# Kernel tuning notes

Hardware: AMD Instinct MI355X
Metric: run time of the kernel (lower is better)

The kernel has to match this reference:

```python
import jax, jax.numpy as jnp
import numpy as np

INPUT_DIM = 512
EMBED_DIM = 512
N_HEAD = 8
HEAD_DIM = EMBED_DIM // N_HEAD


def setup_inputs() -> dict:
    key = jax.random.key(0)
    k0, k1, k2 = jax.random.split(key, 3)
    B, S = 2, 4096
    X = jax.random.normal(k0, (B, S, INPUT_DIM), dtype=jnp.float32)
    # xavier_uniform for Linear weights (torch weight shape [out, in])
    def xavier(k, out_f, in_f):
        bound = float(np.sqrt(6.0 / (in_f + out_f)))
        return jax.random.uniform(k, (out_f, in_f), jnp.float32, -bound, bound)
    W_qkv = xavier(k1, 3 * EMBED_DIM, INPUT_DIM)
    b_qkv = jnp.zeros((3 * EMBED_DIM,), jnp.float32)
    W_o = xavier(k2, EMBED_DIM, EMBED_DIM)
    b_o = jnp.zeros((EMBED_DIM,), jnp.float32)
    return {"X": X, "W_qkv": W_qkv, "b_qkv": b_qkv, "W_o": W_o, "b_o": b_o}


def reference(X, W_qkv, b_qkv, W_o, b_o):
    B, S, _ = X.shape
    # fused QKV projection: [B,S,3E]
    qkv = jnp.einsum("bsd,ed->bse", X, W_qkv) + b_qkv
    # [B,S,H,3*hd] -> [B,H,S,3*hd]
    qkv = qkv.reshape(B, S, N_HEAD, 3 * HEAD_DIM).transpose(0, 2, 1, 3)
    q, k, v = jnp.split(qkv, 3, axis=-1)
    scale = 1.0 / jnp.sqrt(jnp.asarray(HEAD_DIM, q.dtype))
    logits = jnp.einsum("bhqd,bhkd->bhqk", q, k) * scale  # [B,H,S,S]
    attn = jax.nn.softmax(logits, axis=-1)
    vals = jnp.einsum("bhqk,bhkd->bhqd", attn, v)
    vals = vals.transpose(0, 2, 1, 3).reshape(B, S, EMBED_DIM)
    out = jnp.einsum("bse,fe->bsf", vals, W_o) + b_o
    return out
```

## Files before the change

kernel.cpp:

```cpp
#include <hip/hip_runtime.h>

#define S_   4096
#define D_IN 512
#define E_   512
#define HD   64

typedef __attribute__((ext_vector_type(8))) short short8;
typedef __attribute__((ext_vector_type(16))) float f32x16;

#define MFMA32(a, b, c) __builtin_amdgcn_mfma_f32_32x32x16_bf16((a), (b), (c), 0, 0, 0)

__device__ __forceinline__ unsigned short f2bf(float f) {
  unsigned u = __builtin_bit_cast(unsigned, f);
  u = (u + 0x7FFFu + ((u >> 16) & 1u)) >> 16;
  return (unsigned short)u;
}

__device__ __forceinline__ unsigned cvt_pk_bf16(float lo, float hi) {
  unsigned r;
  asm("v_cvt_pk_bf16_f32 %0, %1, %2" : "=v"(r) : "v"(lo), "v"(hi));
  return r;
}

__device__ __forceinline__ f32x16 splat16(float x) {
  f32x16 v;
#pragma unroll
  for (int i = 0; i < 16; ++i) v[i] = x;
  return v;
}

__global__ __launch_bounds__(256) void cvt3(const float* __restrict__ X,
                                            const float* __restrict__ Wq,
                                            const float* __restrict__ Wo,
                                            unsigned short* __restrict__ Xb,
                                            unsigned short* __restrict__ Wqb,
                                            unsigned short* __restrict__ Wob) {
  int bid = blockIdx.x;
  const float* src;
  unsigned short* dst;
  int i;
  if (bid < 4096)      { src = X;  dst = Xb;  i = bid * 256 + threadIdx.x; }
  else if (bid < 4864) { src = Wq; dst = Wqb; i = (bid - 4096) * 256 + threadIdx.x; }
  else                 { src = Wo; dst = Wob; i = (bid - 4864) * 256 + threadIdx.x; }
  float4 v = reinterpret_cast<const float4*>(src)[i];
  ushort4 o;
  o.x = f2bf(v.x); o.y = f2bf(v.y); o.z = f2bf(v.z); o.w = f2bf(v.w);
  reinterpret_cast<ushort4*>(dst)[i] = o;
}

__global__ __launch_bounds__(256, 3) void qkv_proj(const unsigned short* __restrict__ Xb,
                                                   const unsigned short* __restrict__ Wb,
                                                   const float* __restrict__ bias,
                                                   unsigned short* __restrict__ Qb,
                                                   unsigned short* __restrict__ Kb,
                                                   unsigned short* __restrict__ Vt) {
  __shared__ unsigned short Al[128][72];
  __shared__ unsigned short Bl[128][72];
  const int tid = threadIdx.x;
  const int w = tid >> 6, l = tid & 63, h = l >> 5, r31 = l & 31;
  const int wm = w >> 1, wn = w & 1;
  const int m0 = blockIdx.x * 128, n0 = blockIdx.y * 128;
  const int sr = tid >> 1, sc = tid & 1;

  f32x16 a00 = {}, a01 = {}, a10 = {}, a11 = {};
  const unsigned short* ap = Xb + (size_t)(m0 + sr) * D_IN + sc * 32;
  const unsigned short* bp = Wb + (size_t)(n0 + sr) * D_IN + sc * 32;
  for (int k0 = 0; k0 < D_IN; k0 += 64) {
    int4 av0 = *reinterpret_cast<const int4*>(ap + k0);
    int4 av1 = *reinterpret_cast<const int4*>(ap + k0 + 8);
    int4 av2 = *reinterpret_cast<const int4*>(ap + k0 + 16);
    int4 av3 = *reinterpret_cast<const int4*>(ap + k0 + 24);
    int4 bv0 = *reinterpret_cast<const int4*>(bp + k0);
    int4 bv1 = *reinterpret_cast<const int4*>(bp + k0 + 8);
    int4 bv2 = *reinterpret_cast<const int4*>(bp + k0 + 16);
    int4 bv3 = *reinterpret_cast<const int4*>(bp + k0 + 24);
    __syncthreads();
    *reinterpret_cast<int4*>(&Al[sr][sc * 32])      = av0;
    *reinterpret_cast<int4*>(&Al[sr][sc * 32 + 8])  = av1;
    *reinterpret_cast<int4*>(&Al[sr][sc * 32 + 16]) = av2;
    *reinterpret_cast<int4*>(&Al[sr][sc * 32 + 24]) = av3;
    *reinterpret_cast<int4*>(&Bl[sr][sc * 32])      = bv0;
    *reinterpret_cast<int4*>(&Bl[sr][sc * 32 + 8])  = bv1;
    *reinterpret_cast<int4*>(&Bl[sr][sc * 32 + 16]) = bv2;
    *reinterpret_cast<int4*>(&Bl[sr][sc * 32 + 24]) = bv3;
    __syncthreads();
#pragma unroll
    for (int c = 0; c < 4; ++c) {
      short8 aA = *reinterpret_cast<const short8*>(&Al[wm * 64 + r31][c * 16 + h * 8]);
      short8 aB = *reinterpret_cast<const short8*>(&Al[wm * 64 + 32 + r31][c * 16 + h * 8]);
      short8 bA = *reinterpret_cast<const short8*>(&Bl[wn * 64 + r31][c * 16 + h * 8]);
      short8 bB = *reinterpret_cast<const short8*>(&Bl[wn * 64 + 32 + r31][c * 16 + h * 8]);
      a00 = MFMA32(aA, bA, a00);
      a01 = MFMA32(aA, bB, a01);
      a10 = MFMA32(aB, bA, a10);
      a11 = MFMA32(aB, bB, a11);
    }
  }
#pragma unroll
  for (int rb = 0; rb < 2; ++rb)
#pragma unroll
    for (int cb = 0; cb < 2; ++cb) {
      const f32x16 A = rb ? (cb ? a11 : a10) : (cb ? a01 : a00);
      int n = n0 + wn * 64 + cb * 32 + r31;
      int hh = n / 192;
      int j = n - hh * 192;
      int t3 = j >> 6;
      int d = j & 63;
      float bn = bias[n];
      int mbase0 = m0 + wm * 64 + rb * 32 + h * 4;
#pragma unroll
      for (int rq = 0; rq < 4; ++rq) {
        int mb = mbase0 + rq * 8;
        int bb = mb >> 12;
        int ssb = mb & 4095;
        int bhh = bb * 8 + hh;
        if (t3 == 0) {
#pragma unroll
          for (int i = 0; i < 4; ++i)
            Qb[((size_t)bhh * S_ + ssb + i) * HD + d] =
                f2bf((A[rq * 4 + i] + bn) * (0.125f * 1.44269504088896f));
        } else if (t3 == 1) {
#pragma unroll
          for (int i = 0; i < 4; ++i)
            Kb[((size_t)bhh * S_ + ssb + i) * HD + d] = f2bf(A[rq * 4 + i] + bn);
        } else {
          int sp = (ssb & ~12) | ((ssb & 8) >> 1) | ((ssb & 4) << 1);
          ushort4 o;
          o.x = f2bf(A[rq * 4 + 0] + bn);
          o.y = f2bf(A[rq * 4 + 1] + bn);
          o.z = f2bf(A[rq * 4 + 2] + bn);
          o.w = f2bf(A[rq * 4 + 3] + bn);
          *reinterpret_cast<ushort4*>(&Vt[((size_t)bhh * HD + d) * S_ + sp]) = o;
        }
      }
    }
}

__global__ __launch_bounds__(512, 4) void attn_fwd(const unsigned short* __restrict__ Qb,
                                                   const unsigned short* __restrict__ Kb,
                                                   const unsigned short* __restrict__ Vt,
                                                   unsigned short* __restrict__ vals) {
  __shared__ char smem[73728];
  const int tid = threadIdx.x;
  const int w = tid >> 6, l = tid & 63, h = l >> 5, r31 = l & 31;
  const int grp = w >> 2;
  const int wq = w & 3;
  const int bh = blockIdx.x >> 5;
  const int q0 = (blockIdx.x & 31) * 128;
  const int lt256 = tid & 255;
  const int sr = lt256 >> 2, sc = lt256 & 3;

  unsigned short (*Kl)[64][72] =
      reinterpret_cast<unsigned short(*)[64][72]>(smem + grp * 36864);
  unsigned short (*Vl)[64][72] =
      reinterpret_cast<unsigned short(*)[64][72]>(smem + grp * 36864 + 18432);

  const int qrow = q0 + wq * 32 + r31;
  const unsigned short* qp = Qb + ((size_t)bh * S_ + qrow) * HD + h * 8;
  short8 bq[4];
#pragma unroll
  for (int c = 0; c < 4; ++c)
    bq[c] = *reinterpret_cast<const short8*>(qp + c * 16);

  f32x16 po0 = {}, po1 = {};
  float lacc = 0.f;

  const int kvbase = grp * 2048;
  const unsigned short* kptr = Kb + ((size_t)bh * S_ + kvbase + sr) * HD + sc * 16;
  const unsigned short* vptr = Vt + ((size_t)bh * HD + sr) * S_ + kvbase + sc * 16;

  {
    int4 kA = *reinterpret_cast<const int4*>(kptr);
    int4 kB = *reinterpret_cast<const int4*>(kptr + 8);
    int4 vA = *reinterpret_cast<const int4*>(vptr);
    int4 vB = *reinterpret_cast<const int4*>(vptr + 8);
    *reinterpret_cast<int4*>(&Kl[0][sr][sc * 16])     = kA;
    *reinterpret_cast<int4*>(&Kl[0][sr][sc * 16 + 8]) = kB;
    *reinterpret_cast<int4*>(&Vl[0][sr][sc * 16])     = vA;
    *reinterpret_cast<int4*>(&Vl[0][sr][sc * 16 + 8]) = vB;
  }
  __syncthreads();

  for (int kt = 0; kt < 32; ++kt) {
    const int cur = kt & 1;
    int4 kA, kB, vA, vB;
    if (kt < 31) {
      const unsigned short* kp = kptr + (size_t)(kt + 1) * 64 * HD;
      const unsigned short* vp = vptr + (kt + 1) * 64;
      kA = *reinterpret_cast<const int4*>(kp);
      kB = *reinterpret_cast<const int4*>(kp + 8);
      vA = *reinterpret_cast<const int4*>(vp);
      vB = *reinterpret_cast<const int4*>(vp + 8);
    }

    f32x16 s0 = splat16(-16.f), s1 = splat16(-16.f);
#pragma unroll
    for (int c = 0; c < 4; ++c) {
      short8 k0 = *reinterpret_cast<const short8*>(&Kl[cur][r31][c * 16 + h * 8]);
      s0 = MFMA32(k0, bq[c], s0);
      short8 k1 = *reinterpret_cast<const short8*>(&Kl[cur][32 + r31][c * 16 + h * 8]);
      s1 = MFMA32(k1, bq[c], s1);
    }

#pragma unroll
    for (int i = 0; i < 16; ++i) {
      s0[i] = __builtin_amdgcn_exp2f(s0[i]);
      s1[i] = __builtin_amdgcn_exp2f(s1[i]);
    }
    float r0 = ((s0[0] + s0[1]) + (s0[2] + s0[3])) + ((s0[4] + s0[5]) + (s0[6] + s0[7]));
    float r1 = ((s0[8] + s0[9]) + (s0[10] + s0[11])) + ((s0[12] + s0[13]) + (s0[14] + s0[15]));
    float r2 = ((s1[0] + s1[1]) + (s1[2] + s1[3])) + ((s1[4] + s1[5]) + (s1[6] + s1[7]));
    float r3 = ((s1[8] + s1[9]) + (s1[10] + s1[11])) + ((s1[12] + s1[13]) + (s1[14] + s1[15]));
    lacc += (r0 + r1) + (r2 + r3);

#pragma unroll
    for (int c = 0; c < 4; ++c) {
      const f32x16 pp = (c < 2) ? s0 : s1;
      const int o8 = (c & 1) * 8;
      uint4 pk;
      pk.x = cvt_pk_bf16(pp[o8 + 0], pp[o8 + 1]);
      pk.y = cvt_pk_bf16(pp[o8 + 2], pp[o8 + 3]);
      pk.z = cvt_pk_bf16(pp[o8 + 4], pp[o8 + 5]);
      pk.w = cvt_pk_bf16(pp[o8 + 6], pp[o8 + 7]);
      short8 pf = __builtin_bit_cast(short8, pk);
      short8 v0 = *reinterpret_cast<const short8*>(&Vl[cur][r31][c * 16 + h * 8]);
      po0 = MFMA32(v0, pf, po0);
      short8 v1 = *reinterpret_cast<const short8*>(&Vl[cur][32 + r31][c * 16 + h * 8]);
      po1 = MFMA32(v1, pf, po1);
    }

    if (kt < 31) {
      *reinterpret_cast<int4*>(&Kl[cur ^ 1][sr][sc * 16])     = kA;
      *reinterpret_cast<int4*>(&Kl[cur ^ 1][sr][sc * 16 + 8]) = kB;
      *reinterpret_cast<int4*>(&Vl[cur ^ 1][sr][sc * 16])     = vA;
      *reinterpret_cast<int4*>(&Vl[cur ^ 1][sr][sc * 16 + 8]) = vB;
    }
    __syncthreads();
  }

  float ltp = lacc + __shfl_xor(lacc, 32);
  float* Ox = reinterpret_cast<float*>(smem);
  float* lx = reinterpret_cast<float*>(smem + 34816);
  const int qlocal = wq * 32 + r31;
  if (grp == 0) {
#pragma unroll
    for (int db = 0; db < 2; ++db) {
      const f32x16 P = db ? po1 : po0;
#pragma unroll
      for (int rq = 0; rq < 4; ++rq) {
        float4 st = {P[rq * 4 + 0], P[rq * 4 + 1], P[rq * 4 + 2], P[rq * 4 + 3]};
        *reinterpret_cast<float4*>(&Ox[qlocal * 68 + db * 32 + rq * 8 + h * 4]) = st;
      }
    }
    if (h == 0) lx[qlocal] = ltp;
  }
  __syncthreads();
  if (grp == 1) {
    float inv = 1.0f / (ltp + lx[qlocal]);
    const int b = bh >> 3, hd = bh & 7;
    unsigned short* op = vals + ((size_t)b * S_ + qrow) * E_ + hd * HD + h * 4;
#pragma unroll
    for (int db = 0; db < 2; ++db) {
      const f32x16 P = db ? po1 : po0;
#pragma unroll
      for (int rq = 0; rq < 4; ++rq) {
        float4 pv = *reinterpret_cast<const float4*>(&Ox[qlocal * 68 + db * 32 + rq * 8 + h * 4]);
        ushort4 o;
        o.x = f2bf((P[rq * 4 + 0] + pv.x) * inv);
        o.y = f2bf((P[rq * 4 + 1] + pv.y) * inv);
        o.z = f2bf((P[rq * 4 + 2] + pv.z) * inv);
        o.w = f2bf((P[rq * 4 + 3] + pv.w) * inv);
        *reinterpret_cast<ushort4*>(op + db * 32 + rq * 8) = o;
      }
    }
  }
}

__global__ __launch_bounds__(256, 3) void o_proj(const unsigned short* __restrict__ Ab,
                                                 const unsigned short* __restrict__ Wb,
                                                 const float* __restrict__ bias,
                                                 float* __restrict__ out) {
  __shared__ unsigned short Al[128][72];
  __shared__ unsigned short Bl[128][72];
  const int tid = threadIdx.x;
  const int w = tid >> 6, l = tid & 63, h = l >> 5, r31 = l & 31;
  const int wm = w >> 1, wn = w & 1;
  const int m0 = blockIdx.x * 128, n0 = blockIdx.y * 128;
  const int sr = tid >> 1, sc = tid & 1;

  f32x16 a00 = {}, a01 = {}, a10 = {}, a11 = {};
  const unsigned short* ap = Ab + (size_t)(m0 + sr) * E_ + sc * 32;
  const unsigned short* bp = Wb + (size_t)(n0 + sr) * E_ + sc * 32;
  for (int k0 = 0; k0 < E_; k0 += 64) {
    int4 av0 = *reinterpret_cast<const int4*>(ap + k0);
    int4 av1 = *reinterpret_cast<const int4*>(ap + k0 + 8);
    int4 av2 = *reinterpret_cast<const int4*>(ap + k0 + 16);
    int4 av3 = *reinterpret_cast<const int4*>(ap + k0 + 24);
    int4 bv0 = *reinterpret_cast<const int4*>(bp + k0);
    int4 bv1 = *reinterpret_cast<const int4*>(bp + k0 + 8);
    int4 bv2 = *reinterpret_cast<const int4*>(bp + k0 + 16);
    int4 bv3 = *reinterpret_cast<const int4*>(bp + k0 + 24);
    __syncthreads();
    *reinterpret_cast<int4*>(&Al[sr][sc * 32])      = av0;
    *reinterpret_cast<int4*>(&Al[sr][sc * 32 + 8])  = av1;
    *reinterpret_cast<int4*>(&Al[sr][sc * 32 + 16]) = av2;
    *reinterpret_cast<int4*>(&Al[sr][sc * 32 + 24]) = av3;
    *reinterpret_cast<int4*>(&Bl[sr][sc * 32])      = bv0;
    *reinterpret_cast<int4*>(&Bl[sr][sc * 32 + 8])  = bv1;
    *reinterpret_cast<int4*>(&Bl[sr][sc * 32 + 16]) = bv2;
    *reinterpret_cast<int4*>(&Bl[sr][sc * 32 + 24]) = bv3;
    __syncthreads();
#pragma unroll
    for (int c = 0; c < 4; ++c) {
      short8 aA = *reinterpret_cast<const short8*>(&Al[wm * 64 + r31][c * 16 + h * 8]);
      short8 aB = *reinterpret_cast<const short8*>(&Al[wm * 64 + 32 + r31][c * 16 + h * 8]);
      short8 bA = *reinterpret_cast<const short8*>(&Bl[wn * 64 + r31][c * 16 + h * 8]);
      short8 bB = *reinterpret_cast<const short8*>(&Bl[wn * 64 + 32 + r31][c * 16 + h * 8]);
      a00 = MFMA32(aA, bA, a00);
      a01 = MFMA32(aA, bB, a01);
      a10 = MFMA32(aB, bA, a10);
      a11 = MFMA32(aB, bB, a11);
    }
  }
#pragma unroll
  for (int rb = 0; rb < 2; ++rb)
#pragma unroll
    for (int cb = 0; cb < 2; ++cb) {
      const f32x16 A = rb ? (cb ? a11 : a10) : (cb ? a01 : a00);
      int n = n0 + wn * 64 + cb * 32 + r31;
      float bn = bias[n];
      int mbase0 = m0 + wm * 64 + rb * 32 + h * 4;
#pragma unroll
      for (int rq = 0; rq < 4; ++rq)
#pragma unroll
        for (int i = 0; i < 4; ++i)
          out[(size_t)(mbase0 + rq * 8 + i) * E_ + n] = A[rq * 4 + i] + bn;
    }
}

extern "C" void kernel_launch(void* const* d_in, const int* in_sizes, int n_in,
                              void* d_out, int out_size, void* d_ws, size_t ws_size,
                              hipStream_t stream) {
  const float* X    = (const float*)d_in[0];
  const float* Wqkv = (const float*)d_in[1];
  const float* bqkv = (const float*)d_in[2];
  const float* Wo   = (const float*)d_in[3];
  const float* bo   = (const float*)d_in[4];
  float* out = (float*)d_out;

  char* ws = (char*)d_ws;
  unsigned short* Xb   = (unsigned short*)(ws);
  unsigned short* Wqb  = (unsigned short*)(ws + 8388608);
  unsigned short* Wob  = (unsigned short*)(ws + 9961472);
  unsigned short* Qb   = (unsigned short*)(ws + 10485760);
  unsigned short* Kb   = (unsigned short*)(ws + 18874368);
  unsigned short* Vt   = (unsigned short*)(ws + 27262976);
  unsigned short* vals = (unsigned short*)(ws + 35651584);

  cvt3<<<5120, 256, 0, stream>>>(X, Wqkv, Wo, Xb, Wqb, Wob);
  qkv_proj<<<dim3(64, 12), 256, 0, stream>>>(Xb, Wqb, bqkv, Qb, Kb, Vt);
  attn_fwd<<<512, 512, 0, stream>>>(Qb, Kb, Vt, vals);
  o_proj<<<dim3(64, 4), 256, 0, stream>>>(vals, Wob, bo, out);
}
```

Measured before the change: 126.0 us.

## Fuse X bf16 conversion into QKV GEMM, swizzle attention blocks, interleave exp with PV MFMAs

Drops the separate X fp32→bf16 conversion pass and instead has the QKV projection load fp32 X and convert it in registers before writing to LDS. This removes one 8 MB write and one 8 MB read round trip, at the cost of twice the global load bytes for X inside the GEMM, which reloads X across 12 column blocks. The attention kernel also remaps block indices so consecutive blocks hit different (batch, head) pairs. It splits the exp and PV MFMA work into two halves wrapped in s_setprio to overlap transcendental and matrix work.

```diff
diff --git a/kernel.cpp b/kernel.cpp
--- a/kernel.cpp
+++ b/kernel.cpp
@@ -29,26 +29,23 @@
   return v;
 }
 
-__global__ __launch_bounds__(256) void cvt3(const float* __restrict__ X,
-                                            const float* __restrict__ Wq,
-                                            const float* __restrict__ Wo,
-                                            unsigned short* __restrict__ Xb,
-                                            unsigned short* __restrict__ Wqb,
-                                            unsigned short* __restrict__ Wob) {
+__global__ __launch_bounds__(256) void cvt_w(const float* __restrict__ Wq,
+                                             const float* __restrict__ Wo,
+                                             unsigned short* __restrict__ Wqb,
+                                             unsigned short* __restrict__ Wob) {
   int bid = blockIdx.x;
   const float* src;
   unsigned short* dst;
   int i;
-  if (bid < 4096)      { src = X;  dst = Xb;  i = bid * 256 + threadIdx.x; }
-  else if (bid < 4864) { src = Wq; dst = Wqb; i = (bid - 4096) * 256 + threadIdx.x; }
-  else                 { src = Wo; dst = Wob; i = (bid - 4864) * 256 + threadIdx.x; }
+  if (bid < 768) { src = Wq; dst = Wqb; i = bid * 256 + threadIdx.x; }
+  else           { src = Wo; dst = Wob; i = (bid - 768) * 256 + threadIdx.x; }
   float4 v = reinterpret_cast<const float4*>(src)[i];
   ushort4 o;
   o.x = f2bf(v.x); o.y = f2bf(v.y); o.z = f2bf(v.z); o.w = f2bf(v.w);
   reinterpret_cast<ushort4*>(dst)[i] = o;
 }
 
-__global__ __launch_bounds__(256, 3) void qkv_proj(const unsigned short* __restrict__ Xb,
+__global__ __launch_bounds__(256, 3) void qkv_proj(const float* __restrict__ Xf,
                                                    const unsigned short* __restrict__ Wb,
                                                    const float* __restrict__ bias,
                                                    unsigned short* __restrict__ Qb,
@@ -63,22 +60,28 @@
   const int sr = tid >> 1, sc = tid & 1;
 
   f32x16 a00 = {}, a01 = {}, a10 = {}, a11 = {};
-  const unsigned short* ap = Xb + (size_t)(m0 + sr) * D_IN + sc * 32;
-  const unsigned short* bp = Wb + (size_t)(n0 + sr) * D_IN + sc * 32;
+  const float*          apf = Xf + (size_t)(m0 + sr) * D_IN + sc * 32;
+  const unsigned short* bp  = Wb + (size_t)(n0 + sr) * D_IN + sc * 32;
   for (int k0 = 0; k0 < D_IN; k0 += 64) {
-    int4 av0 = *reinterpret_cast<const int4*>(ap + k0);
-    int4 av1 = *reinterpret_cast<const int4*>(ap + k0 + 8);
-    int4 av2 = *reinterpret_cast<const int4*>(ap + k0 + 16);
-    int4 av3 = *reinterpret_cast<const int4*>(ap + k0 + 24);
+    float4 af[8];
+#pragma unroll
+    for (int j = 0; j < 8; ++j)
+      af[j] = *reinterpret_cast<const float4*>(apf + k0 + j * 4);
     int4 bv0 = *reinterpret_cast<const int4*>(bp + k0);
     int4 bv1 = *reinterpret_cast<const int4*>(bp + k0 + 8);
     int4 bv2 = *reinterpret_cast<const int4*>(bp + k0 + 16);
     int4 bv3 = *reinterpret_cast<const int4*>(bp + k0 + 24);
-    __syncthreads();
-    *reinterpret_cast<int4*>(&Al[sr][sc * 32])      = av0;
-    *reinterpret_cast<int4*>(&Al[sr][sc * 32 + 8])  = av1;
-    *reinterpret_cast<int4*>(&Al[sr][sc * 32 + 16]) = av2;
-    *reinterpret_cast<int4*>(&Al[sr][sc * 32 + 24]) = av3;
+    ushort4 ac[8];
+#pragma unroll
+    for (int j = 0; j < 8; ++j) {
+      ac[j].x = f2bf(af[j].x); ac[j].y = f2bf(af[j].y);
+      ac[j].z = f2bf(af[j].z); ac[j].w = f2bf(af[j].w);
+    }
+    __syncthreads();
+#pragma unroll
+    for (int j = 0; j < 4; ++j)
+      *reinterpret_cast<int4*>(&Al[sr][sc * 32 + j * 8]) =
+          *reinterpret_cast<const int4*>(&ac[j * 2]);
     *reinterpret_cast<int4*>(&Bl[sr][sc * 32])      = bv0;
     *reinterpret_cast<int4*>(&Bl[sr][sc * 32 + 8])  = bv1;
     *reinterpret_cast<int4*>(&Bl[sr][sc * 32 + 16]) = bv2;
@@ -145,8 +148,9 @@
   const int w = tid >> 6, l = tid & 63, h = l >> 5, r31 = l & 31;
   const int grp = w >> 2;
   const int wq = w & 3;
-  const int bh = blockIdx.x >> 5;
-  const int q0 = (blockIdx.x & 31) * 128;
+  const int swz = (blockIdx.x & 7) * 64 + (blockIdx.x >> 3);
+  const int bh = swz >> 5;
+  const int q0 = (swz & 31) * 128;
   const int lt256 = tid & 255;
   const int sr = lt256 >> 2, sc = lt256 & 3;
 
@@ -194,6 +198,7 @@
     }
 
     f32x16 s0 = splat16(-16.f), s1 = splat16(-16.f);
+    __builtin_amdgcn_s_setprio(1);
 #pragma unroll
     for (int c = 0; c < 4; ++c) {
       short8 k0 = *reinterpret_cast<const short8*>(&Kl[cur][r31][c * 16 + h * 8]);
@@ -201,33 +206,51 @@
       short8 k1 = *reinterpret_cast<const short8*>(&Kl[cur][32 + r31][c * 16 + h * 8]);
       s1 = MFMA32(k1, bq[c], s1);
     }
-
-#pragma unroll
-    for (int i = 0; i < 16; ++i) {
-      s0[i] = __builtin_amdgcn_exp2f(s0[i]);
-      s1[i] = __builtin_amdgcn_exp2f(s1[i]);
-    }
+    __builtin_amdgcn_s_setprio(0);
+
+#pragma unroll
+    for (int i = 0; i < 16; ++i) s0[i] = __builtin_amdgcn_exp2f(s0[i]);
+    __builtin_amdgcn_s_setprio(1);
+#pragma unroll
+    for (int c = 0; c < 2; ++c) {
+      const int o8 = (c & 1) * 8;
+      uint4 pk;
+      pk.x = cvt_pk_bf16(s0[o8 + 0], s0[o8 + 1]);
+      pk.y = cvt_pk_bf16(s0[o8 + 2], s0[o8 + 3]);
+      pk.z = cvt_pk_bf16(s0[o8 + 4], s0[o8 + 5]);
+      pk.w = cvt_pk_bf16(s0[o8 + 6], s0[o8 + 7]);
+      short8 pf = __builtin_bit_cast(short8, pk);
+      short8 v0 = *reinterpret_cast<const short8*>(&Vl[cur][r31][c * 16 + h * 8]);
+      po0 = MFMA32(v0, pf, po0);
+      short8 v1 = *reinterpret_cast<const short8*>(&Vl[cur][32 + r31][c * 16 + h * 8]);
+      po1 = MFMA32(v1, pf, po1);
+    }
+    __builtin_amdgcn_s_setprio(0);
+
+#pragma unroll
+    for (int i = 0; i < 16; ++i) s1[i] = __builtin_amdgcn_exp2f(s1[i]);
+    __builtin_amdgcn_s_setprio(1);
+#pragma unroll
+    for (int c = 2; c < 4; ++c) {
+      const int o8 = (c & 1) * 8;
+      uint4 pk;
+      pk.x = cvt_pk_bf16(s1[o8 + 0], s1[o8 + 1]);
+      pk.y = cvt_pk_bf16(s1[o8 + 2], s1[o8 + 3]);
+      pk.z = cvt_pk_bf16(s1[o8 + 4], s1[o8 + 5]);
+      pk.w = cvt_pk_bf16(s1[o8 + 6], s1[o8 + 7]);
+      short8 pf = __builtin_bit_cast(short8, pk);
+      short8 v0 = *reinterpret_cast<const short8*>(&Vl[cur][r31][c * 16 + h * 8]);
+      po0 = MFMA32(v0, pf, po0);
+      short8 v1 = *reinterpret_cast<const short8*>(&Vl[cur][32 + r31][c * 16 + h * 8]);
+      po1 = MFMA32(v1, pf, po1);
+    }
+    __builtin_amdgcn_s_setprio(0);
+
     float r0 = ((s0[0] + s0[1]) + (s0[2] + s0[3])) + ((s0[4] + s0[5]) + (s0[6] + s0[7]));
     float r1 = ((s0[8] + s0[9]) + (s0[10] + s0[11])) + ((s0[12] + s0[13]) + (s0[14] + s0[15]));
     float r2 = ((s1[0] + s1[1]) + (s1[2] + s1[3])) + ((s1[4] + s1[5]) + (s1[6] + s1[7]));
     float r3 = ((s1[8] + s1[9]) + (s1[10] + s1[11])) + ((s1[12] + s1[13]) + (s1[14] + s1[15]));
     lacc += (r0 + r1) + (r2 + r3);
-
-#pragma unroll
-    for (int c = 0; c < 4; ++c) {
-      const f32x16 pp = (c < 2) ? s0 : s1;
-      const int o8 = (c & 1) * 8;
-      uint4 pk;
-      pk.x = cvt_pk_bf16(pp[o8 + 0], pp[o8 + 1]);
-      pk.y = cvt_pk_bf16(pp[o8 + 2], pp[o8 + 3]);
-      pk.z = cvt_pk_bf16(pp[o8 + 4], pp[o8 + 5]);
-      pk.w = cvt_pk_bf16(pp[o8 + 6], pp[o8 + 7]);
-      short8 pf = __builtin_bit_cast(short8, pk);
-      short8 v0 = *reinterpret_cast<const short8*>(&Vl[cur][r31][c * 16 + h * 8]);
-      po0 = MFMA32(v0, pf, po0);
-      short8 v1 = *reinterpret_cast<const short8*>(&Vl[cur][32 + r31][c * 16 + h * 8]);
-      po1 = MFMA32(v1, pf, po1);
-    }
 
     if (kt < 31) {
       *reinterpret_cast<int4*>(&Kl[cur ^ 1][sr][sc * 16])     = kA;
@@ -349,7 +372,6 @@
   float* out = (float*)d_out;
 
   char* ws = (char*)d_ws;
-  unsigned short* Xb   = (unsigned short*)(ws);
   unsigned short* Wqb  = (unsigned short*)(ws + 8388608);
   unsigned short* Wob  = (unsigned short*)(ws + 9961472);
   unsigned short* Qb   = (unsigned short*)(ws + 10485760);
@@ -357,8 +379,8 @@
   unsigned short* Vt   = (unsigned short*)(ws + 27262976);
   unsigned short* vals = (unsigned short*)(ws + 35651584);
 
-  cvt3<<<5120, 256, 0, stream>>>(X, Wqkv, Wo, Xb, Wqb, Wob);
-  qkv_proj<<<dim3(64, 12), 256, 0, stream>>>(Xb, Wqb, bqkv, Qb, Kb, Vt);
+  cvt_w<<<1024, 256, 0, stream>>>(Wqkv, Wo, Wqb, Wob);
+  qkv_proj<<<dim3(64, 12), 256, 0, stream>>>(X, Wqb, bqkv, Qb, Kb, Vt);
   attn_fwd<<<512, 512, 0, stream>>>(Qb, Kb, Vt, vals);
   o_proj<<<dim3(64, 4), 256, 0, stream>>>(vals, Wob, bo, out);
 }
```

Measured after the change: 429.7 us. +240.9%, slower.
